# Optimization experiments

Hardware: AMD Instinct MI355X
Metric: run time of the kernel (lower is better)

Reference implementation:

```python
import jax, jax.numpy as jnp
import numpy as np
import math

NFEAT = 1024
NHID = 512
NLAYERS = 8
LAMDA = 0.5
ALPHA = 0.1
N_DIA = 48
DIA_L = 64
N = N_DIA * DIA_L


def setup_inputs() -> dict:
    key = jax.random.key(0)
    ks = jax.random.split(key, 16)
    stdv_fc = 1.0 / math.sqrt(NFEAT)
    stdv_gc = 1.0 / math.sqrt(NHID)
    inp = {
        'a': jax.random.normal(ks[0], (N, NFEAT), jnp.float32),
        'v': jax.random.normal(ks[1], (N, NFEAT), jnp.float32),
        'l': jax.random.normal(ks[2], (N, NFEAT), jnp.float32),
        'W0': jax.random.uniform(ks[3], (NFEAT, NHID), jnp.float32, -stdv_fc, stdv_fc),
        'b0': jax.random.uniform(ks[4], (NHID,), jnp.float32, -stdv_fc, stdv_fc),
        'W1': jax.random.uniform(ks[5], (NFEAT, NHID), jnp.float32, -stdv_fc, stdv_fc),
        'b1': jax.random.uniform(ks[6], (NHID,), jnp.float32, -stdv_fc, stdv_fc),
        'W2': jax.random.uniform(ks[7], (NFEAT, NHID), jnp.float32, -stdv_fc, stdv_fc),
        'b2': jax.random.uniform(ks[8], (NHID,), jnp.float32, -stdv_fc, stdv_fc),
        'Wconv': jax.random.uniform(ks[9], (NLAYERS, NHID, NHID), jnp.float32, -stdv_gc, stdv_gc),
        'dia_len': DIA_L,  # uniform dialogue length
        'topicLabel': jnp.zeros((N,), jnp.int64),
    }
    return inp


def create_big_adj(a, v, l, dia_l):
    n = a.shape[0]
    d = n // dia_l
    feats = jnp.stack([a, v, l])                    # [3, N, F]
    x = feats.reshape(3, d, dia_l, -1)              # [3, D, L, F]
    nrm = x / jnp.sqrt(jnp.sum(x * x, axis=-1, keepdims=True))
    cos = jnp.einsum('mdif,mdjf->mdij', nrm, nrm) * 0.99999
    sim = jnp.arccos(cos)                           # [3, D, L, L]
    adj = jnp.zeros((3 * n, 3 * n), dtype=a.dtype)
    base = jnp.arange(d)[:, None, None] * dia_l     # dialogue start offsets
    rows = jnp.broadcast_to(base + jnp.arange(dia_l)[:, None], (d, dia_l, dia_l))
    cols = jnp.broadcast_to(base + jnp.arange(dia_l)[None, :], (d, dia_l, dia_l))
    for m in range(3):  # same-modality block-diagonal acos-similarity blocks
        adj = adj.at[m * n + rows, m * n + cols].set(sim[m])
    k = jnp.arange(n)
    for m in range(3):  # cross-modal: same-utterance links set to 0.99999
        for mm in range(3):
            if m != mm:
                adj = adj.at[m * n + k, mm * n + k].set(0.99999)
    dsum = jnp.sum(adj, axis=1)
    dinv = dsum ** -0.5
    return dinv[:, None] * adj * dinv[None, :]


def reference(a, v, l, W0, b0, W1, b1, W2, b2, Wconv, dia_len, topicLabel):
    relu = jax.nn.relu
    # eval mode: dropout is identity
    a_ = relu(a @ W0 + b0)
    l_ = relu(l @ W1 + b1)
    v_ = relu(v @ W2 + b2)
    x = jnp.concatenate([a_, v_, l_], axis=0)       # [3N, nhidden]
    adj = create_big_adj(a, v, l, dia_len)
    h0 = x
    h = x
    for i in range(NLAYERS):
        theta = math.log(LAMDA / (i + 1) + 1.0)
        hi = adj @ h
        support = (1.0 - ALPHA) * hi + ALPHA * h0
        h = relu(theta * (support @ Wconv[i]) + (1.0 - theta) * support)
    n = a.shape[0]
    out = jnp.concatenate([h[:n], h[n:2 * n], h[2 * n:]], axis=-1)  # [N, 3*nhidden]
    out = jnp.concatenate([l, out], axis=-1)        # use_residue
    return out
```

## Files before the change

kernel.cpp:

```cpp
#include <hip/hip_runtime.h>
#include <hip/hip_bf16.h>
#include <cmath>

#define NFEAT 1024
#define NHID  512
#define NLAYERS 8
#define NDIA 48
#define DIAL 64
#define NROW (NDIA*DIAL)
#define NROW3 (3*NROW)

typedef short bf16x8 __attribute__((ext_vector_type(8)));
typedef float f32x4  __attribute__((ext_vector_type(4)));
typedef unsigned short u16x8 __attribute__((ext_vector_type(8)));
typedef unsigned short u16x4 __attribute__((ext_vector_type(4)));
typedef unsigned short ushort_t;

__device__ __forceinline__ unsigned short f2bf(float x) {
  __hip_bfloat16 h = __float2bfloat16(x);
  return __builtin_bit_cast(unsigned short, h);
}
__device__ __forceinline__ float bf2f(unsigned short u) {
  __hip_bfloat16 h = __builtin_bit_cast(__hip_bfloat16, u);
  return __bfloat162float(h);
}

__device__ __forceinline__ void gload16(const void* g, void* l) {
  __builtin_amdgcn_global_load_lds(
      (const __attribute__((address_space(1))) void*)g,
      (__attribute__((address_space(3))) void*)l, 16, 0, 0);
}

__global__ __launch_bounds__(256) void k_prep(const float* __restrict__ a, const float* __restrict__ v,
                      const float* __restrict__ l, ushort_t* __restrict__ Abuf,
                      ushort_t* __restrict__ Xn) {
  int gid = blockIdx.x * 256 + threadIdx.x;
  int row = gid >> 6, lane = gid & 63;
  int m = row / NROW, r = row % NROW;
  const float* src = (m == 0 ? a : (m == 1 ? v : l)) + (size_t)r * NFEAT;
  float4 x[4];
  float s = 0.f;
#pragma unroll
  for (int q = 0; q < 4; ++q) {
    x[q] = *reinterpret_cast<const float4*>(src + lane * 4 + q * 256);
    s += x[q].x*x[q].x + x[q].y*x[q].y + x[q].z*x[q].z + x[q].w*x[q].w;
  }
#pragma unroll
  for (int off = 32; off; off >>= 1) s += __shfl_xor(s, off);
  float inv = rsqrtf(s);
  ushort_t* da = Abuf + (size_t)row * NFEAT;
  ushort_t* dn = Xn + (size_t)row * NFEAT;
#pragma unroll
  for (int q = 0; q < 4; ++q) {
    u16x4 oa, on;
    oa[0] = f2bf(x[q].x); oa[1] = f2bf(x[q].y); oa[2] = f2bf(x[q].z); oa[3] = f2bf(x[q].w);
    on[0] = f2bf(x[q].x * inv); on[1] = f2bf(x[q].y * inv);
    on[2] = f2bf(x[q].z * inv); on[3] = f2bf(x[q].w * inv);
    *reinterpret_cast<u16x4*>(da + lane * 4 + q * 256) = oa;
    *reinterpret_cast<u16x4*>(dn + lane * 4 + q * 256) = on;
  }
}

__global__ __launch_bounds__(256) void k_simm(const ushort_t* __restrict__ Xn,
                      ushort_t* __restrict__ Sbf, float* __restrict__ dinv) {
  __shared__ short Xs[2][4096];
  __shared__ float simS[64][73];
  int blk = blockIdx.x;
  const ushort_t* Xb = Xn + (size_t)blk * 64 * NFEAT;
  int t = threadIdx.x, w = t >> 6, lane = t & 63;
  f32x4 acc[4] = {};

#define STAGE_SIM(b, k0) do { \
    _Pragma("unroll") \
    for (int q = 0; q < 2; ++q) { \
      int f_ = t * 8 + q * 2048; \
      int row_ = f_ >> 6; \
      int col_ = (f_ & 63) ^ ((row_ & 7) << 3); \
      gload16(Xb + (size_t)row_ * NFEAT + (k0) + col_, (void*)(Xs[b] + q * 2048 + w * 512)); \
    } } while (0)

  STAGE_SIM(0, 0);
  __syncthreads();
  for (int it = 0; it < 16; ++it) {
    int cur = it & 1;
    if (it < 15) STAGE_SIM(cur ^ 1, (it + 1) * 64);
    const char* base = (const char*)Xs[cur];
#pragma unroll
    for (int ks = 0; ks < 2; ++ks) {
      int koff = ks * 32 + (lane >> 4) * 8;
      int arow = w * 16 + (lane & 15);
      bf16x8 af = *(const bf16x8*)(base + (((arow << 7) + (koff << 1)) ^ ((arow & 7) << 4)));
#pragma unroll
      for (int j = 0; j < 4; ++j) {
        int brow = j * 16 + (lane & 15);
        bf16x8 bf = *(const bf16x8*)(base + (((brow << 7) + (koff << 1)) ^ ((brow & 7) << 4)));
        acc[j] = __builtin_amdgcn_mfma_f32_16x16x32_bf16(af, bf, acc[j], 0, 0, 0);
      }
    }
    __syncthreads();
  }
#undef STAGE_SIM

#pragma unroll
  for (int j = 0; j < 4; ++j)
#pragma unroll
    for (int e = 0; e < 4; ++e) {
      int r = w * 16 + (lane >> 4) * 4 + e;
      int c = j * 16 + (lane & 15);
      float cc = acc[j][e] * 0.99999f;
      cc = fminf(fmaxf(cc, -0.99999f), 0.99999f);
      simS[r][c] = acosf(cc);
    }
  __syncthreads();
  if (t < 64) {
    float s = 0.f;
#pragma unroll 8
    for (int c = 0; c < 64; ++c) s += simS[t][c];
    float di = rsqrtf(s + 1.99998f);
    simS[t][64] = di;
    dinv[blk * 64 + t] = di;
  }
  __syncthreads();
  ushort_t* Sb = Sbf + (size_t)blk * 4096;
#pragma unroll
  for (int q = 0; q < 2; ++q) {
    int idx = t * 8 + q * 2048;
    int i = idx >> 6, j0 = idx & 63;
    float di = simS[i][64];
    u16x8 o;
#pragma unroll
    for (int e = 0; e < 8; ++e)
      o[e] = f2bf(simS[i][j0 + e] * di * simS[j0 + e][64]);
    *reinterpret_cast<u16x8*>(Sb + idx) = o;
  }
}

__global__ void k_cvt_w(const float* __restrict__ s0, const float* __restrict__ s1,
                        const float* __restrict__ s2, ushort_t* __restrict__ dst,
                        int K, int mode) {
  __shared__ float tile[32][33];
  int z = blockIdx.z;
  const float* src = (mode == 1) ? (s0 + (size_t)z * K * NHID)
                                 : (z == 0 ? s0 : (z == 1 ? s1 : s2));
  ushort_t* d = dst + (size_t)z * NHID * K;
  int n0 = blockIdx.x * 32, k0 = blockIdx.y * 32;
  int tx = threadIdx.x & 31, ty = threadIdx.x >> 5;
#pragma unroll
  for (int q = 0; q < 4; ++q)
    tile[ty + q * 8][tx] = src[(size_t)(k0 + ty + q * 8) * NHID + n0 + tx];
  __syncthreads();
#pragma unroll
  for (int q = 0; q < 4; ++q)
    d[(size_t)(n0 + ty + q * 8) * K + k0 + tx] = f2bf(tile[tx][ty + q * 8]);
}

template<int EPI>
__global__ __launch_bounds__(256) void k_gemm_mfma(
    const ushort_t* __restrict__ A, const ushort_t* __restrict__ B,
    const float* __restrict__ ba, const float* __restrict__ bv, const float* __restrict__ bl,
    const ushort_t* __restrict__ sup, ushort_t* __restrict__ C,
    int K, float theta) {
  __shared__ short As[128 * 64];
  __shared__ short Bs[64 * 64];
  int t = threadIdx.x;
  int w = t >> 6, lane = t & 63;
  int bm = blockIdx.x * 128, bn = blockIdx.y * 64;
  const float* bias = ba;
  if (EPI == 0) {
    int band = bm / NROW;
    B += (size_t)band * NHID * K;
    bias = (band == 0 ? ba : (band == 1 ? bv : bl));
  }
  const ushort_t* Ab = A + (size_t)bm * K;
  const ushort_t* Bb = B + (size_t)bn * K;
  int wr = (w >> 1) * 64, wc = (w & 1) * 32;
  f32x4 acc[4][2] = {};

  for (int k0 = 0; k0 < K; k0 += 64) {
    __syncthreads();
#pragma unroll
    for (int q = 0; q < 4; ++q) {
      int f = t * 8 + q * 2048;
      int row = f >> 6;
      int col = (f & 63) ^ ((row & 7) << 3);
      gload16(Ab + (size_t)row * K + k0 + col, (void*)(As + q * 2048 + w * 512));
    }
#pragma unroll
    for (int q = 0; q < 2; ++q) {
      int f = t * 8 + q * 2048;
      int row = f >> 6;
      int col = (f & 63) ^ ((row & 7) << 3);
      gload16(Bb + (size_t)row * K + k0 + col, (void*)(Bs + q * 2048 + w * 512));
    }
    __syncthreads();
#pragma unroll
    for (int ks = 0; ks < 2; ++ks) {
      bf16x8 af[4], bfr[2];
#pragma unroll
      for (int i = 0; i < 4; ++i) {
        int arow = wr + i * 16 + (lane & 15);
        int ab = (arow << 7) + ((ks * 32 + (lane >> 4) * 8) << 1);
        af[i] = *reinterpret_cast<const bf16x8*>(
            reinterpret_cast<const char*>(As) + (ab ^ ((arow & 7) << 4)));
      }
#pragma unroll
      for (int j = 0; j < 2; ++j) {
        int brow = wc + j * 16 + (lane & 15);
        int bb = (brow << 7) + ((ks * 32 + (lane >> 4) * 8) << 1);
        bfr[j] = *reinterpret_cast<const bf16x8*>(
            reinterpret_cast<const char*>(Bs) + (bb ^ ((brow & 7) << 4)));
      }
#pragma unroll
      for (int i = 0; i < 4; ++i)
#pragma unroll
        for (int j = 0; j < 2; ++j)
          acc[i][j] = __builtin_amdgcn_mfma_f32_16x16x32_bf16(af[i], bfr[j], acc[i][j], 0, 0, 0);
    }
  }
#pragma unroll
  for (int i = 0; i < 4; ++i) {
#pragma unroll
    for (int jf = 0; jf < 2; ++jf) {
      int r0 = bm + wr + i * 16 + (lane >> 4) * 4;
      int c  = bn + wc + jf * 16 + (lane & 15);
#pragma unroll
      for (int j = 0; j < 4; ++j) {
        int r = r0 + j;
        float val = acc[i][jf][j];
        if (EPI == 0) {
          val = fmaxf(val + bias[c], 0.f);
        } else {
          float s = bf2f(sup[(size_t)r * NHID + c]);
          val = fmaxf(theta * val + (1.f - theta) * s, 0.f);
        }
        C[(size_t)r * NHID + c] = f2bf(val);
      }
    }
  }
}

__global__ __launch_bounds__(256) void k_adj(const ushort_t* __restrict__ Sbf,
                      const ushort_t* __restrict__ h, const ushort_t* __restrict__ h0,
                      const float* __restrict__ dinv, ushort_t* __restrict__ sup) {
  __shared__ short Ss[4096];
  __shared__ short Ht[64][72];
  __shared__ float supS[64][76];
  int blk = blockIdx.x, c0 = blockIdx.y * 64;
  int m = blk / NDIA, d = blk % NDIA;
  int t = threadIdx.x, w = t >> 6, lane = t & 63;
  const ushort_t* Sb = Sbf + (size_t)blk * 4096;
#pragma unroll
  for (int q = 0; q < 2; ++q) {
    int f = t * 8 + q * 2048;
    int row = f >> 6;
    int col = (f & 63) ^ ((row & 7) << 3);
    gload16(Sb + row * 64 + col, (void*)(Ss + q * 2048 + w * 512));
  }
  const ushort_t* hb = h + ((size_t)blk * 64) * NHID + c0;
#pragma unroll
  for (int q = 0; q < 2; ++q) {
    int idx = t * 8 + q * 2048;
    int j = idx >> 6, n0 = idx & 63;
    u16x8 hv = *reinterpret_cast<const u16x8*>(hb + (size_t)j * NHID + n0);
#pragma unroll
    for (int e = 0; e < 8; ++e) Ht[n0 + e][j] = hv[e];
  }
  __syncthreads();
  f32x4 acc[4] = {};
#pragma unroll
  for (int ks = 0; ks < 2; ++ks) {
    int koff = ks * 32 + (lane >> 4) * 8;
    int arow = w * 16 + (lane & 15);
    bf16x8 af = *(const bf16x8*)((const char*)Ss + (((arow << 7) + (koff << 1)) ^ ((arow & 7) << 4)));
#pragma unroll
    for (int j = 0; j < 4; ++j) {
      int n = j * 16 + (lane & 15);
      bf16x8 bf = *(const bf16x8*)(&Ht[n][koff]);
      acc[j] = __builtin_amdgcn_mfma_f32_16x16x32_bf16(af, bf, acc[j], 0, 0, 0);
    }
  }
#pragma unroll
  for (int j = 0; j < 4; ++j)
#pragma unroll
    for (int e = 0; e < 4; ++e)
      supS[w * 16 + (lane >> 4) * 4 + e][j * 16 + (lane & 15)] = acc[j][e];
  __syncthreads();
  int r = t >> 2, cc0 = (t & 3) * 16;
  int g = blk * 64 + r;
  int u = d * 64 + r;
  int mm1 = (m + 1) % 3, mm2 = (m + 2) % 3;
  float di = dinv[g];
  float c1 = 0.99999f * di * dinv[mm1 * NROW + u];
  float c2 = 0.99999f * di * dinv[mm2 * NROW + u];
  const ushort_t* p1 = h + ((size_t)mm1 * NROW + u) * NHID + c0 + cc0;
  const ushort_t* p2 = h + ((size_t)mm2 * NROW + u) * NHID + c0 + cc0;
  const ushort_t* pz = h0 + (size_t)g * NHID + c0 + cc0;
  ushort_t* po = sup + (size_t)g * NHID + c0 + cc0;
#pragma unroll
  for (int half = 0; half < 2; ++half) {
    u16x8 h1 = *reinterpret_cast<const u16x8*>(p1 + half * 8);
    u16x8 h2 = *reinterpret_cast<const u16x8*>(p2 + half * 8);
    u16x8 hz = *reinterpret_cast<const u16x8*>(pz + half * 8);
    u16x8 o;
#pragma unroll
    for (int e = 0; e < 8; ++e) {
      float val = 0.9f * (supS[r][cc0 + half * 8 + e] + c1 * bf2f(h1[e]) + c2 * bf2f(h2[e]))
                + 0.1f * bf2f(hz[e]);
      o[e] = f2bf(val);
    }
    *reinterpret_cast<u16x8*>(po + half * 8) = o;
  }
}

__global__ void k_out(const float* __restrict__ l, const ushort_t* __restrict__ h,
                      float* __restrict__ out) {
  int idx = blockIdx.x * blockDim.x + threadIdx.x;
  int i = idx / 640;
  int c4 = (idx % 640) * 4;
  float4 val;
  if (c4 < 1024) {
    val = *reinterpret_cast<const float4*>(l + (size_t)i * NFEAT + c4);
  } else {
    int cc = c4 - 1024;
    int m = cc >> 9, c = cc & 511;
    u16x4 hv = *reinterpret_cast<const u16x4*>(h + ((size_t)m * NROW + i) * NHID + c);
    val.x = bf2f(hv[0]); val.y = bf2f(hv[1]); val.z = bf2f(hv[2]); val.w = bf2f(hv[3]);
  }
  *reinterpret_cast<float4*>(out + (size_t)i * 2560 + c4) = val;
}

extern "C" void kernel_launch(void* const* d_in, const int* in_sizes, int n_in,
                              void* d_out, int out_size, void* d_ws, size_t ws_size,
                              hipStream_t stream) {
  const float* a  = (const float*)d_in[0];
  const float* v  = (const float*)d_in[1];
  const float* l  = (const float*)d_in[2];
  const float* W0 = (const float*)d_in[3];
  const float* b0 = (const float*)d_in[4];
  const float* W1 = (const float*)d_in[5];
  const float* b1 = (const float*)d_in[6];
  const float* W2 = (const float*)d_in[7];
  const float* b2 = (const float*)d_in[8];
  const float* Wc = (const float*)d_in[9];
  float* out = (float*)d_out;

  const size_t SZ = (size_t)NROW3 * NHID;
  const size_t XSZ = (size_t)3 * NROW * NFEAT;
  char* ws = (char*)d_ws;
  ushort_t* Abuf = (ushort_t*)ws;  ws += XSZ * 2;
  ushort_t* Xn   = (ushort_t*)ws;  ws += XSZ * 2;
  ushort_t* h0   = (ushort_t*)ws;  ws += SZ * 2;
  ushort_t* Wtfc = (ushort_t*)ws;  ws += (size_t)3 * NHID * NFEAT * 2;
  ushort_t* Wct  = (ushort_t*)ws;  ws += (size_t)NLAYERS * NHID * NHID * 2;
  ushort_t* Sbf  = (ushort_t*)ws;  ws += (size_t)144 * 4096 * 2;
  float* dinv    = (float*)ws;
  ushort_t* h   = Abuf;
  ushort_t* sup = Xn;

  k_prep<<<NROW3 / 4, 256, 0, stream>>>(a, v, l, Abuf, Xn);
  k_cvt_w<<<dim3(NHID / 32, NFEAT / 32, 3), 256, 0, stream>>>(W0, W2, W1, Wtfc, NFEAT, 0);
  k_cvt_w<<<dim3(NHID / 32, NHID / 32, NLAYERS), 256, 0, stream>>>(Wc, nullptr, nullptr, Wct, NHID, 1);
  k_simm<<<3 * NDIA, 256, 0, stream>>>(Xn, Sbf, dinv);

  k_gemm_mfma<0><<<dim3(NROW3 / 128, NHID / 64), 256, 0, stream>>>(
      Abuf, Wtfc, b0, b2, b1, nullptr, h0, NFEAT, 0.f);

  hipMemcpyAsync(h, h0, SZ * 2, hipMemcpyDeviceToDevice, stream);

  for (int i = 0; i < NLAYERS; ++i) {
    float theta = (float)std::log(0.5 / (i + 1) + 1.0);
    k_adj<<<dim3(3 * NDIA, NHID / 64), 256, 0, stream>>>(Sbf, h, h0, dinv, sup);
    k_gemm_mfma<1><<<dim3(NROW3 / 128, NHID / 64), 256, 0, stream>>>(
        sup, Wct + (size_t)i * NHID * NHID, nullptr, nullptr, nullptr, sup, h, NHID, theta);
  }

  k_out<<<(NROW * 2560 / 4) / 256, 256, 0, stream>>>(l, h, out);
}
```

Measured before the change: 237.6 us.

## Double-buffer GEMM LDS tiles, merge modality blocks in adj kernel, drop h copy

The MFMA GEMM now uses two LDS buffers so the next K tile's global loads are issued while the current tile is computed, with one barrier per step instead of two. The adjacency kernel handles all three modalities of a dialogue in one block, loading the h tiles into LDS once with an XOR swizzle. It still rereads the cross-modal rows from global. The first GEMM writes h0 and h together, which removes the device memcpy. In exchange LDS use and register pressure rise and the adjacency grid has 3x fewer blocks, which may lower occupancy.

```diff
diff --git a/kernel.cpp b/kernel.cpp
--- a/kernel.cpp
+++ b/kernel.cpp
@@ -158,10 +158,10 @@
 __global__ __launch_bounds__(256) void k_gemm_mfma(
     const ushort_t* __restrict__ A, const ushort_t* __restrict__ B,
     const float* __restrict__ ba, const float* __restrict__ bv, const float* __restrict__ bl,
-    const ushort_t* __restrict__ sup, ushort_t* __restrict__ C,
+    const ushort_t* __restrict__ sup, ushort_t* __restrict__ C, ushort_t* __restrict__ C2,
     int K, float theta) {
-  __shared__ short As[128 * 64];
-  __shared__ short Bs[64 * 64];
+  __shared__ short As[2][128 * 64];
+  __shared__ short Bs[2][64 * 64];
   int t = threadIdx.x;
   int w = t >> 6, lane = t & 63;
   int bm = blockIdx.x * 128, bn = blockIdx.y * 64;
@@ -176,39 +176,41 @@
   int wr = (w >> 1) * 64, wc = (w & 1) * 32;
   f32x4 acc[4][2] = {};
 
-  for (int k0 = 0; k0 < K; k0 += 64) {
-    __syncthreads();
-#pragma unroll
-    for (int q = 0; q < 4; ++q) {
-      int f = t * 8 + q * 2048;
-      int row = f >> 6;
-      int col = (f & 63) ^ ((row & 7) << 3);
-      gload16(Ab + (size_t)row * K + k0 + col, (void*)(As + q * 2048 + w * 512));
-    }
-#pragma unroll
-    for (int q = 0; q < 2; ++q) {
-      int f = t * 8 + q * 2048;
-      int row = f >> 6;
-      int col = (f & 63) ^ ((row & 7) << 3);
-      gload16(Bb + (size_t)row * K + k0 + col, (void*)(Bs + q * 2048 + w * 512));
-    }
-    __syncthreads();
+#define STAGE_G(b, k0) do { \
+    _Pragma("unroll") \
+    for (int q = 0; q < 4; ++q) { \
+      int f_ = t * 8 + q * 2048; int row_ = f_ >> 6; \
+      int col_ = (f_ & 63) ^ ((row_ & 7) << 3); \
+      gload16(Ab + (size_t)row_ * K + (k0) + col_, (void*)(As[b] + q * 2048 + w * 512)); } \
+    _Pragma("unroll") \
+    for (int q = 0; q < 2; ++q) { \
+      int f_ = t * 8 + q * 2048; int row_ = f_ >> 6; \
+      int col_ = (f_ & 63) ^ ((row_ & 7) << 3); \
+      gload16(Bb + (size_t)row_ * K + (k0) + col_, (void*)(Bs[b] + q * 2048 + w * 512)); } \
+  } while (0)
+
+  STAGE_G(0, 0);
+  __syncthreads();
+  int T = K >> 6;
+  for (int s = 0; s < T; ++s) {
+    int cur = s & 1;
+    if (s + 1 < T) STAGE_G(cur ^ 1, (s + 1) * 64);
+    const char* ab = (const char*)As[cur];
+    const char* bb = (const char*)Bs[cur];
 #pragma unroll
     for (int ks = 0; ks < 2; ++ks) {
       bf16x8 af[4], bfr[2];
 #pragma unroll
       for (int i = 0; i < 4; ++i) {
         int arow = wr + i * 16 + (lane & 15);
-        int ab = (arow << 7) + ((ks * 32 + (lane >> 4) * 8) << 1);
-        af[i] = *reinterpret_cast<const bf16x8*>(
-            reinterpret_cast<const char*>(As) + (ab ^ ((arow & 7) << 4)));
+        int abo = (arow << 7) + ((ks * 32 + (lane >> 4) * 8) << 1);
+        af[i] = *reinterpret_cast<const bf16x8*>(ab + (abo ^ ((arow & 7) << 4)));
       }
 #pragma unroll
       for (int j = 0; j < 2; ++j) {
         int brow = wc + j * 16 + (lane & 15);
-        int bb = (brow << 7) + ((ks * 32 + (lane >> 4) * 8) << 1);
-        bfr[j] = *reinterpret_cast<const bf16x8*>(
-            reinterpret_cast<const char*>(Bs) + (bb ^ ((brow & 7) << 4)));
+        int bbo = (brow << 7) + ((ks * 32 + (lane >> 4) * 8) << 1);
+        bfr[j] = *reinterpret_cast<const bf16x8*>(bb + (bbo ^ ((brow & 7) << 4)));
       }
 #pragma unroll
       for (int i = 0; i < 4; ++i)
@@ -216,7 +218,10 @@
         for (int j = 0; j < 2; ++j)
           acc[i][j] = __builtin_amdgcn_mfma_f32_16x16x32_bf16(af[i], bfr[j], acc[i][j], 0, 0, 0);
     }
-  }
+    __syncthreads();
+  }
+#undef STAGE_G
+
 #pragma unroll
   for (int i = 0; i < 4; ++i) {
 #pragma unroll
@@ -229,11 +234,14 @@
         float val = acc[i][jf][j];
         if (EPI == 0) {
           val = fmaxf(val + bias[c], 0.f);
+          unsigned short o = f2bf(val);
+          C[(size_t)r * NHID + c] = o;
+          C2[(size_t)r * NHID + c] = o;
         } else {
           float s = bf2f(sup[(size_t)r * NHID + c]);
           val = fmaxf(theta * val + (1.f - theta) * s, 0.f);
+          C[(size_t)r * NHID + c] = f2bf(val);
         }
-        C[(size_t)r * NHID + c] = f2bf(val);
       }
     }
   }
@@ -242,73 +250,84 @@
 __global__ __launch_bounds__(256) void k_adj(const ushort_t* __restrict__ Sbf,
                       const ushort_t* __restrict__ h, const ushort_t* __restrict__ h0,
                       const float* __restrict__ dinv, ushort_t* __restrict__ sup) {
-  __shared__ short Ss[4096];
-  __shared__ short Ht[64][72];
-  __shared__ float supS[64][76];
-  int blk = blockIdx.x, c0 = blockIdx.y * 64;
-  int m = blk / NDIA, d = blk % NDIA;
+  __shared__ short Ss[3 * 4096];
+  __shared__ short Ht[3][64][72];
+  __shared__ float supS[64][69];
+  int d = blockIdx.x, c0 = blockIdx.y * 64;
   int t = threadIdx.x, w = t >> 6, lane = t & 63;
-  const ushort_t* Sb = Sbf + (size_t)blk * 4096;
-#pragma unroll
-  for (int q = 0; q < 2; ++q) {
+#pragma unroll
+  for (int q = 0; q < 6; ++q) {
     int f = t * 8 + q * 2048;
-    int row = f >> 6;
-    int col = (f & 63) ^ ((row & 7) << 3);
-    gload16(Sb + row * 64 + col, (void*)(Ss + q * 2048 + w * 512));
-  }
-  const ushort_t* hb = h + ((size_t)blk * 64) * NHID + c0;
-#pragma unroll
-  for (int q = 0; q < 2; ++q) {
-    int idx = t * 8 + q * 2048;
-    int j = idx >> 6, n0 = idx & 63;
-    u16x8 hv = *reinterpret_cast<const u16x8*>(hb + (size_t)j * NHID + n0);
-#pragma unroll
-    for (int e = 0; e < 8; ++e) Ht[n0 + e][j] = hv[e];
-  }
-  __syncthreads();
-  f32x4 acc[4] = {};
-#pragma unroll
-  for (int ks = 0; ks < 2; ++ks) {
-    int koff = ks * 32 + (lane >> 4) * 8;
-    int arow = w * 16 + (lane & 15);
-    bf16x8 af = *(const bf16x8*)((const char*)Ss + (((arow << 7) + (koff << 1)) ^ ((arow & 7) << 4)));
-#pragma unroll
-    for (int j = 0; j < 4; ++j) {
-      int n = j * 16 + (lane & 15);
-      bf16x8 bf = *(const bf16x8*)(&Ht[n][koff]);
-      acc[j] = __builtin_amdgcn_mfma_f32_16x16x32_bf16(af, bf, acc[j], 0, 0, 0);
-    }
-  }
-#pragma unroll
-  for (int j = 0; j < 4; ++j)
-#pragma unroll
-    for (int e = 0; e < 4; ++e)
-      supS[w * 16 + (lane >> 4) * 4 + e][j * 16 + (lane & 15)] = acc[j][e];
-  __syncthreads();
+    int mod = f >> 12, rem = f & 4095;
+    int row = rem >> 6;
+    int col = (rem & 63) ^ ((row & 7) << 3);
+    gload16(Sbf + ((size_t)(mod * NDIA + d)) * 4096 + row * 64 + col,
+            (void*)(Ss + q * 2048 + w * 512));
+  }
+#pragma unroll
+  for (int q = 0; q < 6; ++q) {
+    int idx = t + q * 256;
+    int mod = idx >> 9, rem = idx & 511;
+    int j = rem >> 3, n0 = (rem & 7) * 8;
+    int key = rem & 7;
+    u16x8 hv = *reinterpret_cast<const u16x8*>(
+        h + ((size_t)(mod * NROW + d * 64 + j)) * NHID + c0 + n0);
+    int js = j ^ (key << 3);
+#pragma unroll
+    for (int e = 0; e < 8; ++e) Ht[mod][n0 + e][js] = hv[e];
+  }
+  __syncthreads();
+  f32x4 acc[3][4] = {};
+#pragma unroll
+  for (int m = 0; m < 3; ++m)
+#pragma unroll
+    for (int ks = 0; ks < 2; ++ks) {
+      int koff = ks * 32 + (lane >> 4) * 8;
+      int arow = w * 16 + (lane & 15);
+      bf16x8 af = *(const bf16x8*)((const char*)Ss + m * 8192 +
+                    (((arow << 7) + (koff << 1)) ^ ((arow & 7) << 4)));
+#pragma unroll
+      for (int j = 0; j < 4; ++j) {
+        int n = j * 16 + (lane & 15);
+        int koff_s = koff ^ (((n >> 3) & 7) << 3);
+        bf16x8 bf = *(const bf16x8*)(&Ht[m][n][koff_s]);
+        acc[m][j] = __builtin_amdgcn_mfma_f32_16x16x32_bf16(af, bf, acc[m][j], 0, 0, 0);
+      }
+    }
   int r = t >> 2, cc0 = (t & 3) * 16;
-  int g = blk * 64 + r;
   int u = d * 64 + r;
-  int mm1 = (m + 1) % 3, mm2 = (m + 2) % 3;
-  float di = dinv[g];
-  float c1 = 0.99999f * di * dinv[mm1 * NROW + u];
-  float c2 = 0.99999f * di * dinv[mm2 * NROW + u];
-  const ushort_t* p1 = h + ((size_t)mm1 * NROW + u) * NHID + c0 + cc0;
-  const ushort_t* p2 = h + ((size_t)mm2 * NROW + u) * NHID + c0 + cc0;
-  const ushort_t* pz = h0 + (size_t)g * NHID + c0 + cc0;
-  ushort_t* po = sup + (size_t)g * NHID + c0 + cc0;
-#pragma unroll
-  for (int half = 0; half < 2; ++half) {
-    u16x8 h1 = *reinterpret_cast<const u16x8*>(p1 + half * 8);
-    u16x8 h2 = *reinterpret_cast<const u16x8*>(p2 + half * 8);
-    u16x8 hz = *reinterpret_cast<const u16x8*>(pz + half * 8);
-    u16x8 o;
-#pragma unroll
-    for (int e = 0; e < 8; ++e) {
-      float val = 0.9f * (supS[r][cc0 + half * 8 + e] + c1 * bf2f(h1[e]) + c2 * bf2f(h2[e]))
-                + 0.1f * bf2f(hz[e]);
-      o[e] = f2bf(val);
-    }
-    *reinterpret_cast<u16x8*>(po + half * 8) = o;
+  float d0 = dinv[u], d1 = dinv[NROW + u], d2 = dinv[2 * NROW + u];
+  float dv[3] = {d0, d1, d2};
+  for (int m = 0; m < 3; ++m) {
+#pragma unroll
+    for (int j = 0; j < 4; ++j)
+#pragma unroll
+      for (int e = 0; e < 4; ++e)
+        supS[w * 16 + (lane >> 4) * 4 + e][j * 16 + (lane & 15)] = acc[m][j][e];
+    __syncthreads();
+    int mm1 = (m + 1) % 3, mm2 = (m + 2) % 3;
+    int g = m * NROW + u;
+    float c1 = 0.99999f * dv[m] * dv[mm1];
+    float c2 = 0.99999f * dv[m] * dv[mm2];
+    const ushort_t* p1 = h + ((size_t)(mm1 * NROW + u)) * NHID + c0 + cc0;
+    const ushort_t* p2 = h + ((size_t)(mm2 * NROW + u)) * NHID + c0 + cc0;
+    const ushort_t* pz = h0 + (size_t)g * NHID + c0 + cc0;
+    ushort_t* po = sup + (size_t)g * NHID + c0 + cc0;
+#pragma unroll
+    for (int half = 0; half < 2; ++half) {
+      u16x8 h1 = *reinterpret_cast<const u16x8*>(p1 + half * 8);
+      u16x8 h2 = *reinterpret_cast<const u16x8*>(p2 + half * 8);
+      u16x8 hz = *reinterpret_cast<const u16x8*>(pz + half * 8);
+      u16x8 o;
+#pragma unroll
+      for (int e = 0; e < 8; ++e) {
+        float val = 0.9f * (supS[r][cc0 + half * 8 + e] + c1 * bf2f(h1[e]) + c2 * bf2f(h2[e]))
+                  + 0.1f * bf2f(hz[e]);
+        o[e] = f2bf(val);
+      }
+      *reinterpret_cast<u16x8*>(po + half * 8) = o;
+    }
+    __syncthreads();
   }
 }
 
@@ -354,8 +373,8 @@
   ushort_t* Wct  = (ushort_t*)ws;  ws += (size_t)NLAYERS * NHID * NHID * 2;
   ushort_t* Sbf  = (ushort_t*)ws;  ws += (size_t)144 * 4096 * 2;
   float* dinv    = (float*)ws;
-  ushort_t* h   = Abuf;
-  ushort_t* sup = Xn;
+  ushort_t* h   = Xn;
+  ushort_t* sup = Xn + SZ;
 
   k_prep<<<NROW3 / 4, 256, 0, stream>>>(a, v, l, Abuf, Xn);
   k_cvt_w<<<dim3(NHID / 32, NFEAT / 32, 3), 256, 0, stream>>>(W0, W2, W1, Wtfc, NFEAT, 0);
@@ -363,15 +382,13 @@
   k_simm<<<3 * NDIA, 256, 0, stream>>>(Xn, Sbf, dinv);
 
   k_gemm_mfma<0><<<dim3(NROW3 / 128, NHID / 64), 256, 0, stream>>>(
-      Abuf, Wtfc, b0, b2, b1, nullptr, h0, NFEAT, 0.f);
-
-  hipMemcpyAsync(h, h0, SZ * 2, hipMemcpyDeviceToDevice, stream);
+      Abuf, Wtfc, b0, b2, b1, nullptr, h0, h, NFEAT, 0.f);
 
   for (int i = 0; i < NLAYERS; ++i) {
     float theta = (float)std::log(0.5 / (i + 1) + 1.0);
-    k_adj<<<dim3(3 * NDIA, NHID / 64), 256, 0, stream>>>(Sbf, h, h0, dinv, sup);
+    k_adj<<<dim3(NDIA, NHID / 64), 256, 0, stream>>>(Sbf, h, h0, dinv, sup);
     k_gemm_mfma<1><<<dim3(NROW3 / 128, NHID / 64), 256, 0, stream>>>(
-        sup, Wct + (size_t)i * NHID * NHID, nullptr, nullptr, nullptr, sup, h, NHID, theta);
+        sup, Wct + (size_t)i * NHID * NHID, nullptr, nullptr, nullptr, sup, h, nullptr, NHID, theta);
   }
 
   k_out<<<(NROW * 2560 / 4) / 256, 256, 0, stream>>>(l, h, out);
```

After: 235.0 us. No clear change (-1.1%).
